# Performance work log

Hardware: AMD Instinct MI355X
Metric: run time of the kernel (lower is better)

The kernel has to match this reference:

```python
import jax, jax.numpy as jnp
import numpy as np

MIN_NORM = 1e-15

# ---- Poincare-ball (c=1) Mobius algebra, matching geoopt pmath ----

def expmap0(u):
    n = jnp.maximum(jnp.linalg.norm(u, axis=-1, keepdims=True), MIN_NORM)
    return jnp.tanh(n) * u / n

def mobius_add(x, y):
    x2 = jnp.sum(x * x, -1, keepdims=True)
    y2 = jnp.sum(y * y, -1, keepdims=True)
    xy = jnp.sum(x * y, -1, keepdims=True)
    num = (1 + 2 * xy + y2) * x + (1 - x2) * y
    den = 1 + 2 * xy + x2 * y2
    return num / jnp.maximum(den, MIN_NORM)

def mobius_matvec(M, x):
    # M: [H, D, D], x: [B, H, D] -> [B, H, D]  (one matvec per ball)
    x_norm = jnp.maximum(jnp.linalg.norm(x, axis=-1, keepdims=True), MIN_NORM)
    mx = jnp.einsum('hij,bhj->bhi', M, x)
    mx_norm = jnp.maximum(jnp.linalg.norm(mx, axis=-1, keepdims=True), MIN_NORM)
    scale = jnp.tanh(mx_norm / x_norm * jnp.arctanh(jnp.minimum(x_norm, 1 - 1e-7)))
    res = scale * mx / mx_norm
    zero_mx = jnp.all(mx == 0, axis=-1, keepdims=True)
    return jnp.where(zero_mx, jnp.zeros_like(res), res)

def hyper_rnn(x_seq, W, U, b):
    # x_seq: [B, S, H, D] -> encodings [B, S, H, D]
    B, S, H, D = x_seq.shape
    h0 = jnp.zeros((B, H, D), x_seq.dtype)
    def step(h, x_t):
        wh = mobius_matvec(W, h)
        ux = mobius_matvec(U, x_t)
        h_new = mobius_add(mobius_add(wh, ux), b)
        return h_new, h_new
    _, out = jax.lax.scan(step, h0, jnp.swapaxes(x_seq, 0, 1))
    return jnp.swapaxes(out, 0, 1)

def poinc_dist_all_labels(enc, label_embed):
    # enc: [B,S,H,D], label_embed: [L,H,D] -> dist [B,S,L,H]
    # dist(x,y) = arccosh(1 + 2||x-y||^2 / ((1-||x||^2)(1-||y||^2)))  (c=1)
    a = jnp.sum(enc * enc, -1)                 # [B,S,H]
    lb = jnp.sum(label_embed * label_embed, -1)  # [L,H]
    dot = jnp.einsum('bshd,lhd->bslh', enc, label_embed)  # [B,S,L,H]
    c2 = jnp.maximum(a[:, :, None, :] + lb[None, None, :, :] - 2 * dot, 0.0)
    denom = (1 - a)[:, :, None, :] * (1 - lb)[None, None, :, :]
    arg = 1 + 2 * c2 / jnp.maximum(denom, MIN_NORM)
    return jnp.arccosh(jnp.maximum(arg, 1 + 1e-7))

def setup_inputs() -> dict:
    key = jax.random.key(0)
    ks = jax.random.split(key, 10)
    B, S, V, L, H, D = 32, 256, 30000, 1024, 4, 64
    k = 1.0 / np.sqrt(D)
    x = jax.random.randint(ks[0], (B, S), 0, V, dtype=jnp.int64) if jax.config.jax_enable_x64 else jax.random.randint(ks[0], (B, S), 0, V, dtype=jnp.int32)
    word_embed = expmap0(0.05 * jax.random.normal(ks[1], (V, H, D), jnp.float32))
    label_embed = expmap0(0.05 * jax.random.normal(ks[2], (L, H, D), jnp.float32))
    W = jax.random.uniform(ks[3], (H, D, D), jnp.float32, -k, k)
    U = jax.random.uniform(ks[4], (H, D, D), jnp.float32, -k, k)
    b = expmap0(0.01 * jax.random.normal(ks[5], (H, D), jnp.float32))
    k1 = 1.0 / np.sqrt(S)
    w1 = jax.random.uniform(ks[6], (S // 2, S), jnp.float32, -k1, k1)
    b1 = jax.random.uniform(ks[7], (S // 2,), jnp.float32, -k1, k1)
    k2 = 1.0 / np.sqrt(S // 2)
    w2 = jax.random.uniform(ks[8], (1, S // 2), jnp.float32, -k2, k2)
    b2 = jax.random.uniform(ks[9], (1,), jnp.float32, -k2, k2)
    return {"x": x, "word_embed": word_embed, "label_embed": label_embed,
            "W": W, "U": U, "b": b, "w1": w1, "b1": b1, "w2": w2, "b2": b2}

def reference(x, word_embed, label_embed, W, U, b, w1, b1, w2, b2):
    we = word_embed[x]                         # [B,S,H,D]
    enc = hyper_rnn(we, W, U, b)               # [B,S,H,D]
    dist = poinc_dist_all_labels(enc, label_embed)  # [B,S,L,H]
    interaction = jnp.transpose(dist.sum(-1), (0, 2, 1))  # [B,L,S]
    h1 = jax.nn.relu(jnp.einsum('bls,fs->blf', interaction, w1) + b1)
    out = (jnp.einsum('blf,of->blo', h1, w2) + b2).squeeze(-1)  # [B,L]
    return out
```

## Files before the change

### kernel.cpp

```cpp
#include <hip/hip_runtime.h>
#include <math.h>

#define MIN_NORM 1e-15f


__device__ __forceinline__ float frcp(float x){ return __builtin_amdgcn_rcpf(x); }
__device__ __forceinline__ float fsqrt(float x){ return __builtin_amdgcn_sqrtf(x); }
__device__ __forceinline__ float fast_atanh(float x){
  return 0.5f * __logf((1.f + x) * frcp(1.f - x));
}
__device__ __forceinline__ float fast_tanh(float y){
  float e = __expf(-2.f * y);
  return (1.f - e) * frcp(1.f + e);
}
__device__ __forceinline__ float rdlane(float v, int l){
  return __int_as_float(__builtin_amdgcn_readlane(__float_as_int(v), l));
}

#define DPPADD(v, ctrl) \
  v += __int_as_float(__builtin_amdgcn_update_dpp(0, __float_as_int(v), ctrl, 0xf, 0xf, false));

__device__ __forceinline__ float wred_b(float v){
  DPPADD(v,0x111) DPPADD(v,0x112) DPPADD(v,0x114) DPPADD(v,0x118)
  DPPADD(v,0x142) DPPADD(v,0x143)
  return __int_as_float(__builtin_amdgcn_readlane(__float_as_int(v), 63));
}
__device__ __forceinline__ void wred3_b(float& v0, float& v1, float& v2){
  DPPADD(v0,0x111) DPPADD(v1,0x111) DPPADD(v2,0x111)
  DPPADD(v0,0x112) DPPADD(v1,0x112) DPPADD(v2,0x112)
  DPPADD(v0,0x114) DPPADD(v1,0x114) DPPADD(v2,0x114)
  DPPADD(v0,0x118) DPPADD(v1,0x118) DPPADD(v2,0x118)
  DPPADD(v0,0x142) DPPADD(v1,0x142) DPPADD(v2,0x142)
  DPPADD(v0,0x143) DPPADD(v1,0x143) DPPADD(v2,0x143)
  v0 = __int_as_float(__builtin_amdgcn_readlane(__float_as_int(v0), 63));
  v1 = __int_as_float(__builtin_amdgcn_readlane(__float_as_int(v1), 63));
  v2 = __int_as_float(__builtin_amdgcn_readlane(__float_as_int(v2), 63));
}

__device__ __forceinline__ float wred(float v){
#pragma unroll
  for(int o=32;o;o>>=1) v += __shfl_xor(v, o, 64);
  return v;
}

#define LDS_FENCE() asm volatile("s_waitcnt lgkmcnt(0)" ::: "memory")

#define MATVEC_RL(RES, WROW, MV) {                                       \
  float a0=0.f,a1=0.f,a2=0.f,a3=0.f,a4=0.f,a5=0.f,a6=0.f,a7=0.f;         \
  _Pragma("unroll")                                                      \
  for(int j=0;j<64;j+=8){                                                \
    a0 = fmaf(rdlane(MV,j  ), (WROW)[j  ], a0);                          \
    a1 = fmaf(rdlane(MV,j+1), (WROW)[j+1], a1);                          \
    a2 = fmaf(rdlane(MV,j+2), (WROW)[j+2], a2);                          \
    a3 = fmaf(rdlane(MV,j+3), (WROW)[j+3], a3);                          \
    a4 = fmaf(rdlane(MV,j+4), (WROW)[j+4], a4);                          \
    a5 = fmaf(rdlane(MV,j+5), (WROW)[j+5], a5);                          \
    a6 = fmaf(rdlane(MV,j+6), (WROW)[j+6], a6);                          \
    a7 = fmaf(rdlane(MV,j+7), (WROW)[j+7], a7);                          \
  }                                                                      \
  RES = ((a0+a1)+(a2+a3)) + ((a4+a5)+(a6+a7));                           \
}

#define MATVEC_RL2(R1, W1, R2, W2, MV) {                                 \
  float a0=0.f,a1=0.f,a2=0.f,a3=0.f, c0=0.f,c1=0.f,c2=0.f,c3=0.f;        \
  _Pragma("unroll")                                                      \
  for(int j=0;j<64;j+=4){                                                \
    float s0 = rdlane(MV,j  ), s1 = rdlane(MV,j+1);                      \
    float s2 = rdlane(MV,j+2), s3 = rdlane(MV,j+3);                      \
    a0 = fmaf(s0,(W1)[j  ],a0); c0 = fmaf(s0,(W2)[j  ],c0);              \
    a1 = fmaf(s1,(W1)[j+1],a1); c1 = fmaf(s1,(W2)[j+1],c1);              \
    a2 = fmaf(s2,(W1)[j+2],a2); c2 = fmaf(s2,(W2)[j+2],c2);              \
    a3 = fmaf(s3,(W1)[j+3],a3); c3 = fmaf(s3,(W2)[j+3],c3);              \
  }                                                                      \
  R1 = (a0+a1)+(a2+a3); R2 = (c0+c1)+(c2+c3);                            \
}

__global__ __launch_bounds__(256) void k_wu(const float* __restrict__ W,
    const float* __restrict__ U, float* __restrict__ WU){
  __shared__ float Ws[64*65];
  __shared__ float Us[64*64];
  const int h = blockIdx.x;
  const int t = threadIdx.x;
#pragma unroll
  for(int k=0;k<16;k+=4){
    float4 w4 = *(const float4*)&W[h*4096 + t*16 + k];
    Ws[(t>>2)*65 + (t&3)*16 + k  ] = w4.x; Ws[(t>>2)*65 + (t&3)*16 + k+1] = w4.y;
    Ws[(t>>2)*65 + (t&3)*16 + k+2] = w4.z; Ws[(t>>2)*65 + (t&3)*16 + k+3] = w4.w;
    *(float4*)&Us[t*16 + k] = *(const float4*)&U[h*4096 + t*16 + k];
  }
  __syncthreads();
  const int i = t>>2, j0 = (t&3)*16;
  float acc[16];
#pragma unroll
  for(int j=0;j<16;j++) acc[j]=0.f;
  for(int k=0;k<64;k++){
    float w = Ws[i*65+k];
#pragma unroll
    for(int j=0;j<16;j++) acc[j] = fmaf(w, Us[k*64+j0+j], acc[j]);
  }
#pragma unroll
  for(int j=0;j<16;j+=4)
    *(float4*)&WU[h*4096 + i*64 + j0 + j] = make_float4(acc[j],acc[j+1],acc[j+2],acc[j+3]);
}

__global__ __launch_bounds__(256) void k_ux(const int* __restrict__ x,
    const float* __restrict__ wemb, const float* __restrict__ U,
    const float* __restrict__ WU, const float* __restrict__ bvec,
    float* __restrict__ ux, float* __restrict__ wux,
    float* __restrict__ uxn2, float* __restrict__ uxb){
  const int wv = threadIdx.x >> 6, lane = threadIdx.x & 63;
  const int h = blockIdx.x & 3;
  const int bs0 = (blockIdx.x >> 2)*32 + wv*8;
  float urow[64], wurow[64];
  const float* Up  = U  + h*4096 + lane*64;
  const float* WUp = WU + h*4096 + lane*64;
#pragma unroll
  for(int j=0;j<64;j+=4){
    float4 a = *(const float4*)(Up + j);
    urow[j]=a.x; urow[j+1]=a.y; urow[j+2]=a.z; urow[j+3]=a.w;
    float4 c = *(const float4*)(WUp + j);
    wurow[j]=c.x; wurow[j+1]=c.y; wurow[j+2]=c.z; wurow[j+3]=c.w;
  }
  const float bi = bvec[h*64 + lane];
  int vv[8];
#pragma unroll
  for(int k=0;k<8;k++) vv[k] = x[bs0+k];
  float xv[8];
#pragma unroll
  for(int k=0;k<8;k++) xv[k] = wemb[(size_t)vv[k]*256 + h*64 + lane];
#pragma unroll 2
  for(int k=0;k<8;k++){
    float mx, wmx;
    MATVEC_RL2(mx, urow, wmx, wurow, xv[k]);
    float t0 = xv[k]*xv[k], t1 = mx*mx, t2 = mx*bi;
    wred3_b(t0, t1, t2);
    float xn  = fmaxf(fsqrt(t0), MIN_NORM);
    float mxn = fmaxf(fsqrt(t1), MIN_NORM);
    float scale = fast_tanh(mxn*frcp(xn) * fast_atanh(fminf(xn, 1.f-1e-7f)));
    float sm = scale * frcp(mxn);
    const int bid = (bs0+k)*4 + h;
    ux [(size_t)bid*64 + lane] = sm * mx;
    wux[(size_t)bid*64 + lane] = sm * wmx;
    if(lane==0){
      uxn2[bid] = (t1 > 0.f) ? scale*scale : 0.f;
      uxb[bid]  = sm * t2;
    }
  }
}

#define RNN_STEP(S, USLOT, WUSLOT, Y2V, UBV) {                           \
  const float U_ = USLOT, WU_ = WUSLOT;                                  \
  const float Y2_ = (Y2V), UB_ = (UBV);                                  \
  if((S) < 254){                                   \
    USLOT  = uxp  [(size_t)((S)+2)*256 + lane];                          \
    WUSLOT = wuxp [(size_t)((S)+2)*256 + lane];                          \
  }                                                                      \
  float p0 = m*m, p1 = m*U_, p2 = m*bi;                                  \
  wred3_b(p0, p1, p2);                                                   \
  float r_; MATVEC_RL(r_, wrow, m);           \
  float xn  = fmaxf(fsqrt(hh), MIN_NORM);                                \
  float mxn = fmaxf(fsqrt(p0), MIN_NORM);                                \
  float at  = fast_atanh(fminf(xn, 1.f-1e-7f));                          \
  float scale = fast_tanh(mxn*frcp(xn)*at);                              \
  float sm  = scale*frcp(mxn);                                           \
  float wx2 = (p0 > 0.f) ? scale*scale : 0.f;                            \
  float xy  = sm*p1;                                                     \
  float A   = 1.f + 2.f*xy + Y2_;                                        \
  float Bc  = 1.f - wx2;                                                 \
  float iden = frcp(fmaxf(1.f + 2.f*xy + wx2*Y2_, MIN_NORM));            \
  float c1 = A*sm*iden, c2 = Bc*iden;                                    \
  float zz = (A*A*wx2 + 2.f*A*Bc*xy + Bc*Bc*Y2_)*iden*iden;              \
  float zb = (A*sm*p2 + Bc*UB_)*iden;                                    \
  float A2 = 1.f + 2.f*zb + bn2v;                                        \
  float B2 = 1.f - zz;                                                   \
  float iden2 = frcp(fmaxf(1.f + 2.f*zb + zz*bn2v, MIN_NORM));           \
  float e  = A2*iden2, ga = B2*iden2;                                    \
  float al = e*c1, be = e*c2;                                            \
  encp[(size_t)(S)*256 + lane] = fmaf(al, m, fmaf(be, U_, ga*bi));       \
  hh = fmaxf(e*e*zz + 2.f*e*ga*zb + ga*ga*bn2v, 0.f);                    \
  m  = fmaf(al, r_, fmaf(be, WU_, ga*wb));                               \
}

#define RNN_BLOCK(BLK, Y2R, UBR)                                         \
  for(int i=0;i<64;i+=2){                                                \
    RNN_STEP((BLK)*64+i,   uA, wuA, rdlane(Y2R, i),   rdlane(UBR, i));   \
    RNN_STEP((BLK)*64+i+1, uB, wuB, rdlane(Y2R, i+1), rdlane(UBR, i+1)); \
  }

__global__ __launch_bounds__(64) void k_rnn(const float* __restrict__ W,
    const float* __restrict__ bvec, const float* __restrict__ ux,
    const float* __restrict__ wux, const float* __restrict__ uxn2,
    const float* __restrict__ uxb, float* __restrict__ enc){
  const int b = blockIdx.x >> 2, h = blockIdx.x & 3;
  const int lane = threadIdx.x;
  float wrow[64];
  const float* Wp = W + h*4096 + lane*64;
#pragma unroll
  for(int j=0;j<64;j+=4){
    float4 w4 = *(const float4*)(Wp + j);
    wrow[j]=w4.x; wrow[j+1]=w4.y; wrow[j+2]=w4.z; wrow[j+3]=w4.w;
  }
  const float bi = bvec[h*64 + lane];
  const float bn2v = wred_b(bi*bi);
  float wb; MATVEC_RL(wb, wrow, bi);
  const float* uxp   = ux   + (size_t)b*65536 + h*64;
  const float* wuxp  = wux  + (size_t)b*65536 + h*64;
  const float* uxn2p = uxn2 + (size_t)b*1024  + h;
  const float* uxbp  = uxb  + (size_t)b*1024  + h;
  float* encp        = enc  + (size_t)b*65536 + h*64;
  float y2r0 = uxn2p[(      lane)*4], ubr0 = uxbp[(      lane)*4];
  float y2r1 = uxn2p[( 64 + lane)*4], ubr1 = uxbp[( 64 + lane)*4];
  float y2r2 = uxn2p[(128 + lane)*4], ubr2 = uxbp[(128 + lane)*4];
  float y2r3 = uxn2p[(192 + lane)*4], ubr3 = uxbp[(192 + lane)*4];
  float uA  = uxp[lane],         wuA = wuxp[lane];
  float uB  = uxp[256+lane],     wuB = wuxp[256+lane];
  float m = 0.f, hh = 0.f;
  RNN_BLOCK(0, y2r0, ubr0)
  RNN_BLOCK(1, y2r1, ubr1)
  RNN_BLOCK(2, y2r2, ubr2)
  RNN_BLOCK(3, y2r3, ubr3)
}

__global__ __launch_bounds__(256) void k_norm2(const float* __restrict__ src,
    float* __restrict__ dst, int nrows){
  const int row = blockIdx.x*4 + (threadIdx.x>>6);
  const int lane = threadIdx.x & 63;
  if(row >= nrows) return;
  float v = src[(size_t)row*64 + lane];
  float n2 = wred(v*v);
  if(lane==0) dst[row] = n2;
}

__device__ __forceinline__ float pdist(float dot, float a, float lb){
  float c2  = fmaxf(a + lb - 2.f*dot, 0.f);
  float iden = frcp(fmaxf((1.f-a)*(1.f-lb), MIN_NORM));
  float y   = fmaxf(2.f*c2*iden, 1e-7f);
  return __logf(1.f + y + fsqrt(y*(2.f+y)));
}

#define LP 68
__global__ __launch_bounds__(256) void k_dist(const float* __restrict__ enc,
    const float* __restrict__ lab, const float* __restrict__ an,
    const float* __restrict__ lbn, float* __restrict__ inter){
  __shared__ __align__(16) float eT[4*16*LP];
  __shared__ __align__(16) float lT[4*16*LP];
  const int bs0 = blockIdx.x*64, l0 = blockIdx.y*64;
  const int t = threadIdx.x;
  const int tr = t>>4, tc = t&15;
  const int ldr = t>>2, ldp = t&3;
  float acc[4][4][4];
#pragma unroll
  for(int h=0;h<4;h++)
#pragma unroll
    for(int i=0;i<4;i++)
#pragma unroll
      for(int j=0;j<4;j++) acc[h][i][j]=0.f;

  for(int c=0;c<4;c++){
    if(c) __syncthreads();
#pragma unroll
    for(int h=0;h<4;h++){
      float4 ev = *(const float4*)&enc[(size_t)(bs0+ldr)*256 + h*64 + c*16 + ldp*4];
      float4 lv = *(const float4*)&lab[(size_t)(l0 +ldr)*256 + h*64 + c*16 + ldp*4];
      int base = (h*16 + ldp*4)*LP + ldr;
      eT[base     ] = ev.x; eT[base+  LP] = ev.y; eT[base+2*LP] = ev.z; eT[base+3*LP] = ev.w;
      lT[base     ] = lv.x; lT[base+  LP] = lv.y; lT[base+2*LP] = lv.z; lT[base+3*LP] = lv.w;
    }
    __syncthreads();
#pragma unroll
    for(int dd=0;dd<16;dd++){
#pragma unroll
      for(int h=0;h<4;h++){
        float4 e4 = *(const float4*)&eT[(h*16+dd)*LP + tr*4];
        float4 l4 = *(const float4*)&lT[(h*16+dd)*LP + tc*4];
        float ee[4] = {e4.x,e4.y,e4.z,e4.w};
        float ll[4] = {l4.x,l4.y,l4.z,l4.w};
#pragma unroll
        for(int i=0;i<4;i++)
#pragma unroll
          for(int j=0;j<4;j++)
            acc[h][i][j] = fmaf(ee[i], ll[j], acc[h][i][j]);
      }
    }
  }
  const int b = bs0 >> 8;
#pragma unroll
  for(int i=0;i<4;i++){
    const int bs = bs0 + tr*4 + i;
    const int s  = bs & 255;
    float4 ah = *(const float4*)&an[(size_t)bs*4];
#pragma unroll
    for(int j=0;j<4;j++){
      const int l = l0 + tc*4 + j;
      float4 lb = *(const float4*)&lbn[(size_t)l*4];
      float d = pdist(acc[0][i][j], ah.x, lb.x)
              + pdist(acc[1][i][j], ah.y, lb.y)
              + pdist(acc[2][i][j], ah.z, lb.z)
              + pdist(acc[3][i][j], ah.w, lb.w);
      inter[((size_t)b*1024 + l)*256 + s] = d;
    }
  }
}

__global__ __launch_bounds__(256) void k_mlp(const float* __restrict__ inter,
    const float* __restrict__ w1, const float* __restrict__ b1,
    const float* __restrict__ w2, const float* __restrict__ b2,
    float* __restrict__ out){
  __shared__ __align__(16) float rows[32*256];
  __shared__ float part[4][16];
  const int b  = blockIdx.x >> 5;
  const int l0 = (blockIdx.x & 31)*32;
  const int t = threadIdx.x;
  const float* ip = inter + ((size_t)b*1024 + l0)*256;
#pragma unroll
  for(int k=0;k<8;k++){
    int idx = k*1024 + t*4;
    *(float4*)&rows[idx] = *(const float4*)&ip[idx];
  }
  __syncthreads();
  const int f = t & 127, g = t >> 7;
  float acc[16];
#pragma unroll
  for(int li=0;li<16;li++) acc[li]=0.f;
  const float* wp = w1 + (size_t)f*256;
  for(int s=0;s<256;s+=4){
    float4 w4 = *(const float4*)&wp[s];
#pragma unroll
    for(int li=0;li<16;li++){
      float4 r4 = *(const float4*)&rows[(g*16+li)*256 + s];
      acc[li] = fmaf(r4.w, w4.w, fmaf(r4.z, w4.z, fmaf(r4.y, w4.y, fmaf(r4.x, w4.x, acc[li]))));
    }
  }
  const float bb1 = b1[f], ww2 = w2[f];
  const int wave = t>>6, lane = t&63;
#pragma unroll
  for(int li=0;li<16;li++){
    float vv = fmaxf(acc[li] + bb1, 0.f) * ww2;
    vv = wred(vv);
    if(lane==0) part[wave][li] = vv;
  }
  __syncthreads();
  if(t < 32){
    int g2 = t>>4, li = t&15;
    out[(size_t)b*1024 + l0 + g2*16 + li] = part[2*g2][li] + part[2*g2+1][li] + b2[0];
  }
}

extern "C" void kernel_launch(void* const* d_in, const int* in_sizes, int n_in,
                              void* d_out, int out_size, void* d_ws, size_t ws_size,
                              hipStream_t stream){
  const int*   x    = (const int*)d_in[0];
  const float* wemb = (const float*)d_in[1];
  const float* lab  = (const float*)d_in[2];
  const float* W    = (const float*)d_in[3];
  const float* U    = (const float*)d_in[4];
  const float* bv   = (const float*)d_in[5];
  const float* w1   = (const float*)d_in[6];
  const float* b1   = (const float*)d_in[7];
  const float* w2   = (const float*)d_in[8];
  const float* b2   = (const float*)d_in[9];
  float* out = (float*)d_out;

  float* ws    = (float*)d_ws;
  float* enc   = ws;
  float* an    = enc + 2097152;
  float* lbn   = an  + 32768;
  float* ux    = lbn + 4096;
  float* uxn2  = ux  + 2097152;
  float* uxb   = uxn2 + 32768;
  float* wux   = uxb + 32768;
  float* WU    = wux + 2097152;
  float* inter = lbn + 4096;

  k_wu   <<<4,    256, 0, stream>>>(W, U, WU);
  k_ux   <<<1024, 256, 0, stream>>>(x, wemb, U, WU, bv, ux, wux, uxn2, uxb);
  k_norm2<<<1024, 256, 0, stream>>>(lab, lbn, 4096);
  k_rnn  <<<128,   64, 0, stream>>>(W, bv, ux, wux, uxn2, uxb, enc);
  k_norm2<<<8192, 256, 0, stream>>>(enc, an, 32768);
  dim3 g3(128, 16);
  k_dist <<<g3,   256, 0, stream>>>(enc, lab, an, lbn, inter);
  k_mlp  <<<1024, 256, 0, stream>>>(inter, w1, b1, w2, b2, out);
}
```

Measured before the change: 384.6 us.

## Split recurrent W matvec across four waves with LDS reduction per step

The sequential RNN kernel now uses four wavefronts per (batch, head) block instead of one. Each wave computes a 16-column slice of the W·h matvec, writes its partial to LDS, and after a barrier every wave sums the four partials and redundantly runs the scalar Mobius update. This shortens the per-step matvec dependency chain on the critical serial path, at the cost of a block barrier plus LDS round trip on each of the 256 steps. The double-buffered rbuf avoids write-after-read hazards between consecutive steps.

```diff
diff --git a/kernel.cpp b/kernel.cpp
--- a/kernel.cpp
+++ b/kernel.cpp
@@ -44,6 +44,7 @@
 }
 
 #define LDS_FENCE() asm volatile("s_waitcnt lgkmcnt(0)" ::: "memory")
+#define CFENCE()    asm volatile("" ::: "memory")
 
 #define MATVEC_RL(RES, WROW, MV) {                                       \
   float a0=0.f,a1=0.f,a2=0.f,a3=0.f,a4=0.f,a5=0.f,a6=0.f,a7=0.f;         \
@@ -148,16 +149,24 @@
   }
 }
 
-#define RNN_STEP(S, USLOT, WUSLOT, Y2V, UBV) {                           \
+#define RNN_STEP4(S, USLOT, WUSLOT, Y2V, UBV, P) {                       \
   const float U_ = USLOT, WU_ = WUSLOT;                                  \
   const float Y2_ = (Y2V), UB_ = (UBV);                                  \
-  if((S) < 254){                                   \
+  if((S) < 254){                            \
     USLOT  = uxp  [(size_t)((S)+2)*256 + lane];                          \
     WUSLOT = wuxp [(size_t)((S)+2)*256 + lane];                          \
   }                                                                      \
+  float rq = 0.f;                             \
+  _Pragma("unroll")                                                      \
+  for(int j=0;j<16;j++) rq = fmaf(rdlane(m, lb+j), wq[j], rq);           \
+  rbuf[P][w][lane] = rq;                                                 \
   float p0 = m*m, p1 = m*U_, p2 = m*bi;                                  \
-  wred3_b(p0, p1, p2);                                                   \
-  float r_; MATVEC_RL(r_, wrow, m);           \
+  wred3_b(p0, p1, p2);                                  \
+  LDS_FENCE();                                 \
+  __builtin_amdgcn_s_barrier();                                          \
+  CFENCE();                                  \
+  float r_ = (rbuf[P][0][lane]+rbuf[P][1][lane])                         \
+           + (rbuf[P][2][lane]+rbuf[P][3][lane]);                        \
   float xn  = fmaxf(fsqrt(hh), MIN_NORM);                                \
   float mxn = fmaxf(fsqrt(p0), MIN_NORM);                                \
   float at  = fast_atanh(fminf(xn, 1.f-1e-7f));                          \
@@ -176,33 +185,44 @@
   float iden2 = frcp(fmaxf(1.f + 2.f*zb + zz*bn2v, MIN_NORM));           \
   float e  = A2*iden2, ga = B2*iden2;                                    \
   float al = e*c1, be = e*c2;                                            \
-  encp[(size_t)(S)*256 + lane] = fmaf(al, m, fmaf(be, U_, ga*bi));       \
+  if(w==0) encp[(size_t)(S)*256 + lane] = fmaf(al, m, fmaf(be, U_, ga*bi)); \
   hh = fmaxf(e*e*zz + 2.f*e*ga*zb + ga*ga*bn2v, 0.f);                    \
   m  = fmaf(al, r_, fmaf(be, WU_, ga*wb));                               \
 }
 
-#define RNN_BLOCK(BLK, Y2R, UBR)                                         \
+#define RNN_BLOCK4(BLK, Y2R, UBR)                                        \
   for(int i=0;i<64;i+=2){                                                \
-    RNN_STEP((BLK)*64+i,   uA, wuA, rdlane(Y2R, i),   rdlane(UBR, i));   \
-    RNN_STEP((BLK)*64+i+1, uB, wuB, rdlane(Y2R, i+1), rdlane(UBR, i+1)); \
-  }
-
-__global__ __launch_bounds__(64) void k_rnn(const float* __restrict__ W,
+    RNN_STEP4((BLK)*64+i,   uA, wuA, rdlane(Y2R, i),   rdlane(UBR, i),   0); \
+    RNN_STEP4((BLK)*64+i+1, uB, wuB, rdlane(Y2R, i+1), rdlane(UBR, i+1), 1); \
+  }
+
+__global__ __launch_bounds__(256) void k_rnn(const float* __restrict__ W,
     const float* __restrict__ bvec, const float* __restrict__ ux,
     const float* __restrict__ wux, const float* __restrict__ uxn2,
     const float* __restrict__ uxb, float* __restrict__ enc){
   const int b = blockIdx.x >> 2, h = blockIdx.x & 3;
-  const int lane = threadIdx.x;
-  float wrow[64];
-  const float* Wp = W + h*4096 + lane*64;
-#pragma unroll
-  for(int j=0;j<64;j+=4){
+  const int t = threadIdx.x;
+  const int w = t >> 6, lane = t & 63;
+  const int lb = w << 4;
+  __shared__ __align__(16) float rbuf[2][4][64];
+  __shared__ __align__(16) float wbs[4][64];
+  float wq[16];
+  const float* Wp = W + h*4096 + lane*64 + lb;
+#pragma unroll
+  for(int j=0;j<16;j+=4){
     float4 w4 = *(const float4*)(Wp + j);
-    wrow[j]=w4.x; wrow[j+1]=w4.y; wrow[j+2]=w4.z; wrow[j+3]=w4.w;
+    wq[j]=w4.x; wq[j+1]=w4.y; wq[j+2]=w4.z; wq[j+3]=w4.w;
   }
   const float bi = bvec[h*64 + lane];
   const float bn2v = wred_b(bi*bi);
-  float wb; MATVEC_RL(wb, wrow, bi);
+  {
+    float acc = 0.f;
+#pragma unroll
+    for(int j=0;j<16;j++) acc = fmaf(rdlane(bi, lb+j), wq[j], acc);
+    wbs[w][lane] = acc;
+  }
+  __syncthreads();
+  const float wb = (wbs[0][lane]+wbs[1][lane]) + (wbs[2][lane]+wbs[3][lane]);
   const float* uxp   = ux   + (size_t)b*65536 + h*64;
   const float* wuxp  = wux  + (size_t)b*65536 + h*64;
   const float* uxn2p = uxn2 + (size_t)b*1024  + h;
@@ -215,10 +235,10 @@
   float uA  = uxp[lane],         wuA = wuxp[lane];
   float uB  = uxp[256+lane],     wuB = wuxp[256+lane];
   float m = 0.f, hh = 0.f;
-  RNN_BLOCK(0, y2r0, ubr0)
-  RNN_BLOCK(1, y2r1, ubr1)
-  RNN_BLOCK(2, y2r2, ubr2)
-  RNN_BLOCK(3, y2r3, ubr3)
+  RNN_BLOCK4(0, y2r0, ubr0)
+  RNN_BLOCK4(1, y2r1, ubr1)
+  RNN_BLOCK4(2, y2r2, ubr2)
+  RNN_BLOCK4(3, y2r3, ubr3)
 }
 
 __global__ __launch_bounds__(256) void k_norm2(const float* __restrict__ src,
@@ -375,7 +395,7 @@
   k_wu   <<<4,    256, 0, stream>>>(W, U, WU);
   k_ux   <<<1024, 256, 0, stream>>>(x, wemb, U, WU, bv, ux, wux, uxn2, uxb);
   k_norm2<<<1024, 256, 0, stream>>>(lab, lbn, 4096);
-  k_rnn  <<<128,   64, 0, stream>>>(W, bv, ux, wux, uxn2, uxb, enc);
+  k_rnn  <<<128,  256, 0, stream>>>(W, bv, ux, wux, uxn2, uxb, enc);
   k_norm2<<<8192, 256, 0, stream>>>(enc, an, 32768);
   dim3 g3(128, 16);
   k_dist <<<g3,   256, 0, stream>>>(enc, lab, an, lbn, inter);
```

Result: slower. 436.0 us (+13.3%).

## Enlarge distance tile to 128x128 per head and emit norms from RNN

Applied to the files above, without the earlier changes.

The distance kernel now computes a 128x128 (sequence-position x label) tile per block with an 8x8 register micro-tile. It processes one head at a time over the full 64-dim depth and accumulates the arccosh distances into per-thread sums, which it writes back as float4 stores. The RNN kernel writes the squared norm of each hidden state directly, so the separate norm kernel launch over the encodings goes away. The goal is more arithmetic per shared-memory load and one fewer pass over the encodings, at the cost of higher register pressure (128 accumulators), fewer blocks (512), and lane-0 scalar stores inside the serial RNN loop.

```diff
diff --git a/kernel.cpp b/kernel.cpp
--- a/kernel.cpp
+++ b/kernel.cpp
@@ -178,6 +178,7 @@
   float al = e*c1, be = e*c2;                                            \
   encp[(size_t)(S)*256 + lane] = fmaf(al, m, fmaf(be, U_, ga*bi));       \
   hh = fmaxf(e*e*zz + 2.f*e*ga*zb + ga*ga*bn2v, 0.f);                    \
+  if(lane==0) anp[(S)*4] = hh;               \
   m  = fmaf(al, r_, fmaf(be, WU_, ga*wb));                               \
 }
 
@@ -190,7 +191,8 @@
 __global__ __launch_bounds__(64) void k_rnn(const float* __restrict__ W,
     const float* __restrict__ bvec, const float* __restrict__ ux,
     const float* __restrict__ wux, const float* __restrict__ uxn2,
-    const float* __restrict__ uxb, float* __restrict__ enc){
+    const float* __restrict__ uxb, float* __restrict__ enc,
+    float* __restrict__ an){
   const int b = blockIdx.x >> 2, h = blockIdx.x & 3;
   const int lane = threadIdx.x;
   float wrow[64];
@@ -208,6 +210,7 @@
   const float* uxn2p = uxn2 + (size_t)b*1024  + h;
   const float* uxbp  = uxb  + (size_t)b*1024  + h;
   float* encp        = enc  + (size_t)b*65536 + h*64;
+  float* anp         = an   + (size_t)b*1024  + h;
   float y2r0 = uxn2p[(      lane)*4], ubr0 = uxbp[(      lane)*4];
   float y2r1 = uxn2p[( 64 + lane)*4], ubr1 = uxbp[( 64 + lane)*4];
   float y2r2 = uxn2p[(128 + lane)*4], ubr2 = uxbp[(128 + lane)*4];
@@ -238,67 +241,70 @@
   return __logf(1.f + y + fsqrt(y*(2.f+y)));
 }
 
-#define LP 68
+#define DR 132
 __global__ __launch_bounds__(256) void k_dist(const float* __restrict__ enc,
     const float* __restrict__ lab, const float* __restrict__ an,
     const float* __restrict__ lbn, float* __restrict__ inter){
-  __shared__ __align__(16) float eT[4*16*LP];
-  __shared__ __align__(16) float lT[4*16*LP];
-  const int bs0 = blockIdx.x*64, l0 = blockIdx.y*64;
+  __shared__ __align__(16) float eT[64*DR];
+  __shared__ __align__(16) float lT[64*DR];
+  const int bs0 = blockIdx.x*128, l0 = blockIdx.y*128;
   const int t = threadIdx.x;
   const int tr = t>>4, tc = t&15;
-  const int ldr = t>>2, ldp = t&3;
-  float acc[4][4][4];
-#pragma unroll
-  for(int h=0;h<4;h++)
-#pragma unroll
-    for(int i=0;i<4;i++)
-#pragma unroll
-      for(int j=0;j<4;j++) acc[h][i][j]=0.f;
-
-  for(int c=0;c<4;c++){
-    if(c) __syncthreads();
-#pragma unroll
-    for(int h=0;h<4;h++){
-      float4 ev = *(const float4*)&enc[(size_t)(bs0+ldr)*256 + h*64 + c*16 + ldp*4];
-      float4 lv = *(const float4*)&lab[(size_t)(l0 +ldr)*256 + h*64 + c*16 + ldp*4];
-      int base = (h*16 + ldp*4)*LP + ldr;
-      eT[base     ] = ev.x; eT[base+  LP] = ev.y; eT[base+2*LP] = ev.z; eT[base+3*LP] = ev.w;
-      lT[base     ] = lv.x; lT[base+  LP] = lv.y; lT[base+2*LP] = lv.z; lT[base+3*LP] = lv.w;
+  const int sr = t>>1, sd0 = (t&1)*32;
+  float dsum[8][8];
+#pragma unroll
+  for(int i=0;i<8;i++)
+#pragma unroll
+    for(int j=0;j<8;j++) dsum[i][j]=0.f;
+
+  for(int h=0;h<4;h++){
+    if(h) __syncthreads();
+    const float* ep = enc + (size_t)(bs0+sr)*256 + h*64 + sd0;
+    const float* lp = lab + (size_t)(l0 +sr)*256 + h*64 + sd0;
+#pragma unroll
+    for(int j=0;j<32;j+=4){
+      float4 ev = *(const float4*)(ep + j);
+      float4 lv = *(const float4*)(lp + j);
+      const int base = (sd0+j)*DR + sr;
+      eT[base     ] = ev.x; eT[base+  DR] = ev.y; eT[base+2*DR] = ev.z; eT[base+3*DR] = ev.w;
+      lT[base     ] = lv.x; lT[base+  DR] = lv.y; lT[base+2*DR] = lv.z; lT[base+3*DR] = lv.w;
     }
     __syncthreads();
-#pragma unroll
-    for(int dd=0;dd<16;dd++){
-#pragma unroll
-      for(int h=0;h<4;h++){
-        float4 e4 = *(const float4*)&eT[(h*16+dd)*LP + tr*4];
-        float4 l4 = *(const float4*)&lT[(h*16+dd)*LP + tc*4];
-        float ee[4] = {e4.x,e4.y,e4.z,e4.w};
-        float ll[4] = {l4.x,l4.y,l4.z,l4.w};
-#pragma unroll
-        for(int i=0;i<4;i++)
-#pragma unroll
-          for(int j=0;j<4;j++)
-            acc[h][i][j] = fmaf(ee[i], ll[j], acc[h][i][j]);
-      }
+    float acc[8][8];
+#pragma unroll
+    for(int i=0;i<8;i++)
+#pragma unroll
+      for(int j=0;j<8;j++) acc[i][j]=0.f;
+    for(int d=0;d<64;d++){
+      float4 e0 = *(const float4*)&eT[d*DR + tr*8];
+      float4 e1 = *(const float4*)&eT[d*DR + tr*8 + 4];
+      float4 f0 = *(const float4*)&lT[d*DR + tc*8];
+      float4 f1 = *(const float4*)&lT[d*DR + tc*8 + 4];
+      float ee[8] = {e0.x,e0.y,e0.z,e0.w,e1.x,e1.y,e1.z,e1.w};
+      float ll[8] = {f0.x,f0.y,f0.z,f0.w,f1.x,f1.y,f1.z,f1.w};
+#pragma unroll
+      for(int i=0;i<8;i++)
+#pragma unroll
+        for(int j=0;j<8;j++)
+          acc[i][j] = fmaf(ee[i], ll[j], acc[i][j]);
     }
-  }
-  const int b = bs0 >> 8;
-#pragma unroll
-  for(int i=0;i<4;i++){
-    const int bs = bs0 + tr*4 + i;
-    const int s  = bs & 255;
-    float4 ah = *(const float4*)&an[(size_t)bs*4];
-#pragma unroll
-    for(int j=0;j<4;j++){
-      const int l = l0 + tc*4 + j;
-      float4 lb = *(const float4*)&lbn[(size_t)l*4];
-      float d = pdist(acc[0][i][j], ah.x, lb.x)
-              + pdist(acc[1][i][j], ah.y, lb.y)
-              + pdist(acc[2][i][j], ah.z, lb.z)
-              + pdist(acc[3][i][j], ah.w, lb.w);
-      inter[((size_t)b*1024 + l)*256 + s] = d;
-    }
+    float ah[8], lb[8];
+#pragma unroll
+    for(int i=0;i<8;i++) ah[i] = an [(size_t)(bs0+tr*8+i)*4 + h];
+#pragma unroll
+    for(int j=0;j<8;j++) lb[j] = lbn[(size_t)(l0 +tc*8+j)*4 + h];
+#pragma unroll
+    for(int i=0;i<8;i++)
+#pragma unroll
+      for(int j=0;j<8;j++)
+        dsum[i][j] += pdist(acc[i][j], ah[i], lb[j]);
+  }
+  const int b = bs0 >> 8, s0 = (bs0 & 255) + tr*8;
+#pragma unroll
+  for(int j=0;j<8;j++){
+    const size_t row = ((size_t)b*1024 + l0 + tc*8 + j)*256;
+    *(float4*)&inter[row + s0    ] = make_float4(dsum[0][j],dsum[1][j],dsum[2][j],dsum[3][j]);
+    *(float4*)&inter[row + s0 + 4] = make_float4(dsum[4][j],dsum[5][j],dsum[6][j],dsum[7][j]);
   }
 }
 
@@ -375,9 +381,8 @@
   k_wu   <<<4,    256, 0, stream>>>(W, U, WU);
   k_ux   <<<1024, 256, 0, stream>>>(x, wemb, U, WU, bv, ux, wux, uxn2, uxb);
   k_norm2<<<1024, 256, 0, stream>>>(lab, lbn, 4096);
-  k_rnn  <<<128,   64, 0, stream>>>(W, bv, ux, wux, uxn2, uxb, enc);
-  k_norm2<<<8192, 256, 0, stream>>>(enc, an, 32768);
-  dim3 g3(128, 16);
+  k_rnn  <<<128,   64, 0, stream>>>(W, bv, ux, wux, uxn2, uxb, enc, an);
+  dim3 g3(64, 8);
   k_dist <<<g3,   256, 0, stream>>>(enc, lab, an, lbn, inter);
   k_mlp  <<<1024, 256, 0, stream>>>(inter, w1, b1, w2, b2, out);
 }
```

Measured after the change: 399.1 us. +3.8%, slower.
